# Performance work log

Measured on AMD Instinct MI355X. Metric: run time of the kernel, lower is better.

Reference implementation:

```python
import jax, jax.numpy as jnp
import numpy as np

B, P, C, SIZE, K = 2, 4096, 64, 128, 8
RADIUS_PX = 1.5
RAD_POW = 2
TAU = 1.0


def setup_inputs() -> dict:
    key = jax.random.key(0)
    k1, k2, k3 = jax.random.split(key, 3)
    xy = jax.random.uniform(k1, (B, P, 2), minval=-1.0, maxval=1.0)
    z = jax.random.uniform(k2, (B, P, 1), minval=0.1, maxval=2.0)
    pts3D = jnp.concatenate([xy, z], axis=-1)          # [B,P,3] NDC points, z>0
    src = jax.random.normal(k3, (B, C, P), dtype=jnp.float32)  # [B,C,P] features
    return {"pts3D": pts3D, "src": src}


def _rasterize_and_composite(pts3D, src):
    # flip x,y as in the original module (pytorch3d NDC: +x left, +y up)
    pts = pts3D * jnp.array([-1.0, -1.0, 1.0], dtype=pts3D.dtype)
    radius = RADIUS_PX / float(SIZE) * 2.0           # NDC radius
    # pixel-center NDC coordinates, [H,W]
    c = 1.0 - 2.0 * (jnp.arange(SIZE, dtype=pts.dtype) + 0.5) / SIZE
    grid_y, grid_x = jnp.meshgrid(c, c, indexing="ij")
    x, y, z = pts[..., 0], pts[..., 1], pts[..., 2]  # each [B,P]
    # squared NDC distance from every pixel to every point: [B,H,W,P]
    dx = grid_x[None, :, :, None] - x[:, None, None, :]
    dy = grid_y[None, :, :, None] - y[:, None, None, :]
    dist2 = dx * dx + dy * dy
    valid = (dist2 < radius * radius) & (z[:, None, None, :] > 0.0)
    zbuf = jnp.where(valid, z[:, None, None, :], jnp.inf)
    # k-buffer: K nearest-in-depth points per pixel
    neg_topz, idx = jax.lax.top_k(-zbuf, K)          # [B,H,W,K]
    points_idx = jnp.where(neg_topz > -jnp.inf, idx, -1)
    dists = jnp.take_along_axis(dist2, idx, axis=-1)  # [B,H,W,K]
    # blending weights
    dist_n = dists / (radius ** RAD_POW)
    alphas = (1.0 - jnp.clip(dist_n, 0.001, 1.0) ** 0.5) ** TAU
    alphas = jnp.where(points_idx >= 0, alphas, 0.0)
    # alpha compositing front-to-back: w_k = a_k * prod_{j<k} (1 - a_j)
    t = jnp.cumprod(1.0 - alphas, axis=-1)
    t_excl = jnp.concatenate([jnp.ones_like(t[..., :1]), t[..., :-1]], axis=-1)
    w = alphas * t_excl                               # [B,H,W,K]
    safe_idx = jnp.clip(points_idx, 0)
    feats = jax.vmap(lambda f, i: f[:, i])(src, safe_idx)  # [B,C,H,W,K]
    out = jnp.einsum("bchwk,bhwk->bchw", feats, w)
    return out, points_idx


def reference(pts3D, src):
    out, points_idx = _rasterize_and_composite(pts3D, src)
    # background mask: nearest slot empty, dilated by 3x3 max filter
    bg = (points_idx[..., 0] < 0).astype(jnp.float32)  # [B,H,W]
    bg = jax.lax.reduce_window(bg, -jnp.inf, jax.lax.max, (1, 3, 3), (1, 1, 1), "SAME") > 0
    return out, bg
```

## Files before the change

### kernel.cpp

```cpp
#include <hip/hip_runtime.h>
#include <math.h>

#define BB 2
#define PP 4096
#define CC 64
#define SZ 128
#define KK 8

#define R2f 0.00054931640625f
#define SLOTS 16
#define CG 16

typedef unsigned long long u64;
#define EMPTYK (~0ull)

__global__ __launch_bounds__(256) void prep_kernel(const float* __restrict__ pts,
                                                   const float* __restrict__ src,
                                                   float* __restrict__ srcT,
                                                   int* __restrict__ cnt,
                                                   u64* __restrict__ keys) {
    const int tidb = threadIdx.x;
    const int blk  = blockIdx.x;

    {
        const int t  = blk * 256 + tidb;
        const int r  = t & 3;
        const int gp = t >> 2;
        const int b  = gp >> 12;
        const int p  = gp & (PP - 1);
        const float px = pts[(size_t)gp * 3 + 0];
        const float py = pts[(size_t)gp * 3 + 1];
        const float pz = pts[(size_t)gp * 3 + 2];
        if (pz > 0.0f) {
            const float u = (1.0f + px) * 64.0f - 0.5f;
            const float v = (1.0f + py) * 64.0f - 0.5f;
            const int wlo = max(0,   (int)ceilf (u - 1.53f));
            const int whi = min(127, (int)floorf(u + 1.53f));
            const int hlo = max(0,   (int)ceilf (v - 1.53f));
            const int hhi = min(127, (int)floorf(v + 1.53f));
            const int h = hlo + r;
            if (h <= hhi && wlo <= whi) {
                const float gy  = 1.0f - (2 * h + 1) * (1.0f / 128.0f);
                const float dy  = __fadd_rn(gy, py);
                const float dy2 = __fmul_rn(dy, dy);
                const u64 zkey = ((u64)__float_as_uint(pz) << 32) | (unsigned)p;
                for (int w = wlo; w <= whi; ++w) {
                    const float gx = 1.0f - (2 * w + 1) * (1.0f / 128.0f);
                    const float dx = __fadd_rn(gx, px);
                    const float d2 = __fadd_rn(__fmul_rn(dx, dx), dy2);
                    if (d2 < R2f) {
                        const int pix = (b << 14) | (h << 7) | w;
                        const int pos = atomicAdd(cnt + pix, 1);
                        if (pos < SLOTS) keys[pix * SLOTS + pos] = zkey;
                    }
                }
            }
        }
    }

    __shared__ float lt[64][65];
    const int b2 = blk >> 6;
    const int p0 = (blk & 63) << 6;
    const int rr = tidb >> 6;
    const int cc = tidb & 63;
#pragma unroll
    for (int k = 0; k < 16; ++k) {
        const int c = k * 4 + rr;
        lt[c][cc] = src[(size_t)((b2 * CC + c) << 12 | (p0 + cc))];
    }
    __syncthreads();
#pragma unroll
    for (int k = 0; k < 16; ++k) {
        const int pl = k * 4 + rr;
        srcT[(size_t)(((b2 << 12) | (p0 + pl)) << 6 | cc)] = lt[cc][pl];
    }
}

__global__ __launch_bounds__(256) void selcomp_kernel(const float* __restrict__ pts,
                                                      const float* __restrict__ srcT,
                                                      const int* __restrict__ cnt,
                                                      const u64* __restrict__ keys,
                                                      float* __restrict__ out,
                                                      float* __restrict__ bgout) {
    const int t    = blockIdx.x * 256 + threadIdx.x;
    const int pix  = t & 16383;
    const int cg   = (t >> 14) & 3;
    const int b    = t >> 16;
    const int gpix = (b << 14) | pix;

    int n = cnt[gpix];
    n = (n > SLOTS) ? SLOTS : n;

    u64 kk[KK];
#pragma unroll
    for (int s = 0; s < KK; ++s) kk[s] = EMPTYK;
    for (int j = 0; j < n; ++j) {
        u64 kn = keys[gpix * SLOTS + j];
#pragma unroll
        for (int s = 0; s < KK; ++s) {
            if (kn < kk[s]) { u64 tk = kk[s]; kk[s] = kn; kn = tk; }
        }
    }

    const int w = pix & 127;
    const int h = pix >> 7;
    const float gx = 1.0f - (2 * w + 1) * (1.0f / 128.0f);
    const float gy = 1.0f - (2 * h + 1) * (1.0f / 128.0f);

    float acc[CG];
#pragma unroll
    for (int c = 0; c < CG; ++c) acc[c] = 0.0f;

    float T = 1.0f;
#pragma unroll
    for (int s = 0; s < KK; ++s) {
        if (kk[s] == EMPTYK) break;
        const int id = (int)(kk[s] & 0xffffffffu);
        const float* q = pts + (size_t)((b << 12) + id) * 3;
        const float dx = __fadd_rn(gx, q[0]);
        const float dy = __fadd_rn(gy, q[1]);
        const float d2 = __fadd_rn(__fmul_rn(dx, dx), __fmul_rn(dy, dy));
        float dn = d2 / R2f;
        dn = fminf(fmaxf(dn, 0.001f), 1.0f);
        const float a  = 1.0f - sqrtf(dn);
        const float wt = a * T;
        T = T * (1.0f - a);
        const float* fp = srcT + ((size_t)((b << 12) + id) << 6) + cg * CG;
#pragma unroll
        for (int v4 = 0; v4 < CG / 4; ++v4) {
            const float4 f = *(const float4*)(fp + v4 * 4);
            acc[v4 * 4 + 0] = fmaf(wt, f.x, acc[v4 * 4 + 0]);
            acc[v4 * 4 + 1] = fmaf(wt, f.y, acc[v4 * 4 + 1]);
            acc[v4 * 4 + 2] = fmaf(wt, f.z, acc[v4 * 4 + 2]);
            acc[v4 * 4 + 3] = fmaf(wt, f.w, acc[v4 * 4 + 3]);
        }
    }
#pragma unroll
    for (int c = 0; c < CG; ++c)
        out[((size_t)(b * CC + cg * CG + c) << 14) | pix] = acc[c];

    if (cg == 0) {
        int bgv = 0;
#pragma unroll
        for (int dh = -1; dh <= 1; ++dh)
#pragma unroll
            for (int dw = -1; dw <= 1; ++dw) {
                const int hh = h + dh, ww = w + dw;
                if (hh >= 0 && hh < 128 && ww >= 0 && ww < 128)
                    if (cnt[(b << 14) | (hh << 7) | ww] == 0) bgv = 1;
            }
        bgout[gpix] = bgv ? 1.0f : 0.0f;
    }
}

extern "C" void kernel_launch(void* const* d_in, const int* in_sizes, int n_in,
                              void* d_out, int out_size, void* d_ws, size_t ws_size,
                              hipStream_t stream) {
    const float* pts = (const float*)d_in[0];
    const float* src = (const float*)d_in[1];
    float* out = (float*)d_out;

    const int npix = BB * SZ * SZ;
    char* ws = (char*)d_ws;
    float* srcT = (float*)ws;
    int*   cnt  = (int*)(ws + (size_t)BB * PP * CC * 4);
    u64*   keys = (u64*)(ws + (size_t)BB * PP * CC * 4 + (size_t)npix * 4);

    hipMemsetAsync(cnt, 0, (size_t)npix * 4, stream);
    prep_kernel<<<128, 256, 0, stream>>>(pts, src, srcT, cnt, keys);
    selcomp_kernel<<<(BB * 4 * SZ * SZ) / 256, 256, 0, stream>>>(
        pts, srcT, cnt, keys, out, out + BB * CC * SZ * SZ);
}
```

Before: 27.08 us.

## Replace per-pixel append buffer with atomicMin sorted k-buffer insertion

```diff
diff --git a/kernel.cpp b/kernel.cpp
--- a/kernel.cpp
+++ b/kernel.cpp
@@ -8,98 +8,105 @@
 #define KK 8
 
 #define R2f 0.00054931640625f
-#define SLOTS 16
-#define CG 16
 
 typedef unsigned long long u64;
 #define EMPTYK (~0ull)
 
-__global__ __launch_bounds__(256) void prep_kernel(const float* __restrict__ pts,
-                                                   const float* __restrict__ src,
+__global__ __launch_bounds__(256) void prep_kernel(const float* __restrict__ src,
                                                    float* __restrict__ srcT,
-                                                   int* __restrict__ cnt,
                                                    u64* __restrict__ keys) {
     const int tidb = threadIdx.x;
     const int blk  = blockIdx.x;
+    if (blk < 128) {
+        __shared__ float lt[64][65];
+        const int b2  = blk >> 6;
+        const int p0  = (blk & 63) << 6;
+        const int rr  = tidb >> 6;
+        const int ccl = tidb & 63;
+#pragma unroll
+        for (int k = 0; k < 16; ++k) {
+            const int c = k * 4 + rr;
+            lt[c][ccl] = src[(size_t)((b2 * CC + c) << 12 | (p0 + ccl))];
+        }
+        __syncthreads();
+#pragma unroll
+        for (int k = 0; k < 16; ++k) {
+            const int pl = k * 4 + rr;
+            srcT[(size_t)(((b2 << 12) | (p0 + pl)) << 6 | ccl)] = lt[ccl][pl];
+        }
+    } else {
+        const int base = (blk - 128) * 256 + tidb;
+        for (int i = base; i < BB * SZ * SZ * KK; i += 384 * 256)
+            keys[i] = EMPTYK;
+    }
+}
 
-    {
-        const int t  = blk * 256 + tidb;
-        const int r  = t & 3;
-        const int gp = t >> 2;
-        const int b  = gp >> 12;
-        const int p  = gp & (PP - 1);
-        const float px = pts[(size_t)gp * 3 + 0];
-        const float py = pts[(size_t)gp * 3 + 1];
-        const float pz = pts[(size_t)gp * 3 + 2];
-        if (pz > 0.0f) {
-            const float u = (1.0f + px) * 64.0f - 0.5f;
-            const float v = (1.0f + py) * 64.0f - 0.5f;
-            const int wlo = max(0,   (int)ceilf (u - 1.53f));
-            const int whi = min(127, (int)floorf(u + 1.53f));
-            const int hlo = max(0,   (int)ceilf (v - 1.53f));
-            const int hhi = min(127, (int)floorf(v + 1.53f));
-            const int h = hlo + r;
-            if (h <= hhi && wlo <= whi) {
-                const float gy  = 1.0f - (2 * h + 1) * (1.0f / 128.0f);
-                const float dy  = __fadd_rn(gy, py);
-                const float dy2 = __fmul_rn(dy, dy);
-                const u64 zkey = ((u64)__float_as_uint(pz) << 32) | (unsigned)p;
-                for (int w = wlo; w <= whi; ++w) {
-                    const float gx = 1.0f - (2 * w + 1) * (1.0f / 128.0f);
-                    const float dx = __fadd_rn(gx, px);
-                    const float d2 = __fadd_rn(__fmul_rn(dx, dx), dy2);
-                    if (d2 < R2f) {
-                        const int pix = (b << 14) | (h << 7) | w;
-                        const int pos = atomicAdd(cnt + pix, 1);
-                        if (pos < SLOTS) keys[pix * SLOTS + pos] = zkey;
-                    }
-                }
+__global__ __launch_bounds__(256) void bin_kernel(const float* __restrict__ pts,
+                                                  u64* __restrict__ keys) {
+    const int t  = blockIdx.x * 256 + threadIdx.x;
+    const int r  = t & 3;
+    const int gp = t >> 2;
+    const int b  = gp >> 12;
+    const int p  = gp & (PP - 1);
+    const float px = pts[(size_t)gp * 3 + 0];
+    const float py = pts[(size_t)gp * 3 + 1];
+    const float pz = pts[(size_t)gp * 3 + 2];
+    if (!(pz > 0.0f)) return;
+    const float u = (1.0f + px) * 64.0f - 0.5f;
+    const float v = (1.0f + py) * 64.0f - 0.5f;
+    const int wlo = max(0,   (int)ceilf (u - 1.53f));
+    const int whi = min(127, (int)floorf(u + 1.53f));
+    const int hlo = max(0,   (int)ceilf (v - 1.53f));
+    const int hhi = min(127, (int)floorf(v + 1.53f));
+    const int h = hlo + r;
+    if (h > hhi || wlo > whi) return;
+
+    const float gy  = 1.0f - (2 * h + 1) * (1.0f / 128.0f);
+    const float dy  = __fadd_rn(gy, py);
+    const float dy2 = __fmul_rn(dy, dy);
+    const u64 zkey = ((u64)__float_as_uint(pz) << 32) | (unsigned)p;
+
+    for (int w = wlo; w <= whi; ++w) {
+        const float gx = 1.0f - (2 * w + 1) * (1.0f / 128.0f);
+        const float dx = __fadd_rn(gx, px);
+        const float d2 = __fadd_rn(__fmul_rn(dx, dx), dy2);
+        if (d2 < R2f) {
+            const int pix = (b << 14) | (h << 7) | w;
+            u64 kn = zkey;
+#pragma unroll
+            for (int s = 0; s < KK; ++s) {
+                const u64 old = atomicMin(&keys[(size_t)pix * KK + s], kn);
+                kn = (old > kn) ? old : kn;
+                if (kn == EMPTYK) break;
             }
         }
-    }
-
-    __shared__ float lt[64][65];
-    const int b2 = blk >> 6;
-    const int p0 = (blk & 63) << 6;
-    const int rr = tidb >> 6;
-    const int cc = tidb & 63;
-#pragma unroll
-    for (int k = 0; k < 16; ++k) {
-        const int c = k * 4 + rr;
-        lt[c][cc] = src[(size_t)((b2 * CC + c) << 12 | (p0 + cc))];
-    }
-    __syncthreads();
-#pragma unroll
-    for (int k = 0; k < 16; ++k) {
-        const int pl = k * 4 + rr;
-        srcT[(size_t)(((b2 << 12) | (p0 + pl)) << 6 | cc)] = lt[cc][pl];
     }
 }
 
 __global__ __launch_bounds__(256) void selcomp_kernel(const float* __restrict__ pts,
                                                       const float* __restrict__ srcT,
-                                                      const int* __restrict__ cnt,
                                                       const u64* __restrict__ keys,
                                                       float* __restrict__ out,
                                                       float* __restrict__ bgout) {
-    const int t    = blockIdx.x * 256 + threadIdx.x;
-    const int pix  = t & 16383;
-    const int cg   = (t >> 14) & 3;
-    const int b    = t >> 16;
+    const int blk = blockIdx.x;
+    const int ll  = threadIdx.x & 63;
+    const int cqi = threadIdx.x >> 6;
+    const int cqg = blk & 3;
+    const int pg  = (blk >> 2) & 255;
+    const int b   = blk >> 10;
+    const int cq  = cqg * 4 + cqi;
+    const int pix = pg * 64 + ll;
     const int gpix = (b << 14) | pix;
 
-    int n = cnt[gpix];
-    n = (n > SLOTS) ? SLOTS : n;
-
+    const u64* kp = keys + (size_t)gpix * KK;
     u64 kk[KK];
-#pragma unroll
-    for (int s = 0; s < KK; ++s) kk[s] = EMPTYK;
-    for (int j = 0; j < n; ++j) {
-        u64 kn = keys[gpix * SLOTS + j];
-#pragma unroll
-        for (int s = 0; s < KK; ++s) {
-            if (kn < kk[s]) { u64 tk = kk[s]; kk[s] = kn; kn = tk; }
-        }
+    {
+        const ulonglong2 k0 = *(const ulonglong2*)(kp + 0);
+        const ulonglong2 k1 = *(const ulonglong2*)(kp + 2);
+        const ulonglong2 k2 = *(const ulonglong2*)(kp + 4);
+        const ulonglong2 k3 = *(const ulonglong2*)(kp + 6);
+        kk[0] = k0.x; kk[1] = k0.y; kk[2] = k1.x; kk[3] = k1.y;
+        kk[4] = k2.x; kk[5] = k2.y; kk[6] = k3.x; kk[7] = k3.y;
     }
 
     const int w = pix & 127;
@@ -107,10 +114,7 @@
     const float gx = 1.0f - (2 * w + 1) * (1.0f / 128.0f);
     const float gy = 1.0f - (2 * h + 1) * (1.0f / 128.0f);
 
-    float acc[CG];
-#pragma unroll
-    for (int c = 0; c < CG; ++c) acc[c] = 0.0f;
-
+    float acc0 = 0.0f, acc1 = 0.0f, acc2 = 0.0f, acc3 = 0.0f;
     float T = 1.0f;
 #pragma unroll
     for (int s = 0; s < KK; ++s) {
@@ -125,21 +129,19 @@
         const float a  = 1.0f - sqrtf(dn);
         const float wt = a * T;
         T = T * (1.0f - a);
-        const float* fp = srcT + ((size_t)((b << 12) + id) << 6) + cg * CG;
-#pragma unroll
-        for (int v4 = 0; v4 < CG / 4; ++v4) {
-            const float4 f = *(const float4*)(fp + v4 * 4);
-            acc[v4 * 4 + 0] = fmaf(wt, f.x, acc[v4 * 4 + 0]);
-            acc[v4 * 4 + 1] = fmaf(wt, f.y, acc[v4 * 4 + 1]);
-            acc[v4 * 4 + 2] = fmaf(wt, f.z, acc[v4 * 4 + 2]);
-            acc[v4 * 4 + 3] = fmaf(wt, f.w, acc[v4 * 4 + 3]);
-        }
+        const float4 f = *(const float4*)(srcT + ((size_t)((b << 12) + id) << 6) + cq * 4);
+        acc0 = fmaf(wt, f.x, acc0);
+        acc1 = fmaf(wt, f.y, acc1);
+        acc2 = fmaf(wt, f.z, acc2);
+        acc3 = fmaf(wt, f.w, acc3);
     }
-#pragma unroll
-    for (int c = 0; c < CG; ++c)
-        out[((size_t)(b * CC + cg * CG + c) << 14) | pix] = acc[c];
+    const int c0 = cq * 4;
+    out[((size_t)(b * CC + c0 + 0) << 14) | pix] = acc0;
+    out[((size_t)(b * CC + c0 + 1) << 14) | pix] = acc1;
+    out[((size_t)(b * CC + c0 + 2) << 14) | pix] = acc2;
+    out[((size_t)(b * CC + c0 + 3) << 14) | pix] = acc3;
 
-    if (cg == 0) {
+    if (cqg == 0 && cqi == 0) {
         int bgv = 0;
 #pragma unroll
         for (int dh = -1; dh <= 1; ++dh)
@@ -147,7 +149,8 @@
             for (int dw = -1; dw <= 1; ++dw) {
                 const int hh = h + dh, ww = w + dw;
                 if (hh >= 0 && hh < 128 && ww >= 0 && ww < 128)
-                    if (cnt[(b << 14) | (hh << 7) | ww] == 0) bgv = 1;
+                    if (keys[(size_t)((b << 14) | (hh << 7) | ww) * KK] == EMPTYK)
+                        bgv = 1;
             }
         bgout[gpix] = bgv ? 1.0f : 0.0f;
     }
@@ -159,15 +162,13 @@
     const float* pts = (const float*)d_in[0];
     const float* src = (const float*)d_in[1];
     float* out = (float*)d_out;
+    float* bgout = out + BB * CC * SZ * SZ;
 
-    const int npix = BB * SZ * SZ;
     char* ws = (char*)d_ws;
     float* srcT = (float*)ws;
-    int*   cnt  = (int*)(ws + (size_t)BB * PP * CC * 4);
-    u64*   keys = (u64*)(ws + (size_t)BB * PP * CC * 4 + (size_t)npix * 4);
+    u64*   keys = (u64*)(ws + (size_t)BB * PP * CC * 4);
 
-    hipMemsetAsync(cnt, 0, (size_t)npix * 4, stream);
-    prep_kernel<<<128, 256, 0, stream>>>(pts, src, srcT, cnt, keys);
-    selcomp_kernel<<<(BB * 4 * SZ * SZ) / 256, 256, 0, stream>>>(
-        pts, srcT, cnt, keys, out, out + BB * CC * SZ * SZ);
+    prep_kernel<<<512, 256, 0, stream>>>(src, srcT, keys);
+    bin_kernel<<<(BB * PP * 4) / 256, 256, 0, stream>>>(pts, keys);
+    selcomp_kernel<<<2048, 256, 0, stream>>>(pts, srcT, keys, out, bgout);
 }
```

New measurement: 30.60 us. +13.0%, slower.

## Split prep into separate scatter and transpose blocks, widen composite parallelism

Applied to the files above, without the earlier changes.

```diff
diff --git a/kernel.cpp b/kernel.cpp
--- a/kernel.cpp
+++ b/kernel.cpp
@@ -9,7 +9,6 @@
 
 #define R2f 0.00054931640625f
 #define SLOTS 16
-#define CG 16
 
 typedef unsigned long long u64;
 #define EMPTYK (~0ull)
@@ -22,7 +21,7 @@
     const int tidb = threadIdx.x;
     const int blk  = blockIdx.x;
 
-    {
+    if (blk < 128) {
         const int t  = blk * 256 + tidb;
         const int r  = t & 3;
         const int gp = t >> 2;
@@ -31,48 +30,51 @@
         const float px = pts[(size_t)gp * 3 + 0];
         const float py = pts[(size_t)gp * 3 + 1];
         const float pz = pts[(size_t)gp * 3 + 2];
-        if (pz > 0.0f) {
-            const float u = (1.0f + px) * 64.0f - 0.5f;
-            const float v = (1.0f + py) * 64.0f - 0.5f;
-            const int wlo = max(0,   (int)ceilf (u - 1.53f));
-            const int whi = min(127, (int)floorf(u + 1.53f));
-            const int hlo = max(0,   (int)ceilf (v - 1.53f));
-            const int hhi = min(127, (int)floorf(v + 1.53f));
-            const int h = hlo + r;
-            if (h <= hhi && wlo <= whi) {
-                const float gy  = 1.0f - (2 * h + 1) * (1.0f / 128.0f);
-                const float dy  = __fadd_rn(gy, py);
-                const float dy2 = __fmul_rn(dy, dy);
-                const u64 zkey = ((u64)__float_as_uint(pz) << 32) | (unsigned)p;
-                for (int w = wlo; w <= whi; ++w) {
-                    const float gx = 1.0f - (2 * w + 1) * (1.0f / 128.0f);
-                    const float dx = __fadd_rn(gx, px);
-                    const float d2 = __fadd_rn(__fmul_rn(dx, dx), dy2);
-                    if (d2 < R2f) {
-                        const int pix = (b << 14) | (h << 7) | w;
-                        const int pos = atomicAdd(cnt + pix, 1);
-                        if (pos < SLOTS) keys[pix * SLOTS + pos] = zkey;
-                    }
-                }
+        if (!(pz > 0.0f)) return;
+        const float u = (1.0f + px) * 64.0f - 0.5f;
+        const float v = (1.0f + py) * 64.0f - 0.5f;
+        const int wlo = max(0,   (int)ceilf (u - 1.53f));
+        const int whi = min(127, (int)floorf(u + 1.53f));
+        const int hlo = max(0,   (int)ceilf (v - 1.53f));
+        const int hhi = min(127, (int)floorf(v + 1.53f));
+        const int h = hlo + r;
+        if (h > hhi || wlo > whi) return;
+        const float gy  = 1.0f - (2 * h + 1) * (1.0f / 128.0f);
+        const float dy  = __fadd_rn(gy, py);
+        const float dy2 = __fmul_rn(dy, dy);
+        const u64 zkey = ((u64)__float_as_uint(pz) << 32) | (unsigned)p;
+        for (int w = wlo; w <= whi; ++w) {
+            const float gx = 1.0f - (2 * w + 1) * (1.0f / 128.0f);
+            const float dx = __fadd_rn(gx, px);
+            const float d2 = __fadd_rn(__fmul_rn(dx, dx), dy2);
+            if (d2 < R2f) {
+                const int pix = (b << 14) | (h << 7) | w;
+                const int pos = atomicAdd(cnt + pix, 1);
+                if (pos < SLOTS) keys[(size_t)pix * SLOTS + pos] = zkey;
             }
         }
-    }
-
-    __shared__ float lt[64][65];
-    const int b2 = blk >> 6;
-    const int p0 = (blk & 63) << 6;
-    const int rr = tidb >> 6;
-    const int cc = tidb & 63;
+    } else {
+        __shared__ float lt[32][65];
+        const int tb  = blk - 128;
+        const int b2  = tb >> 7;
+        const int rem = tb & 127;
+        const int p0  = (rem >> 1) << 6;
+        const int c0  = (rem & 1) << 5;
+        const int rr  = tidb >> 6;
+        const int ccl = tidb & 63;
 #pragma unroll
-    for (int k = 0; k < 16; ++k) {
-        const int c = k * 4 + rr;
-        lt[c][cc] = src[(size_t)((b2 * CC + c) << 12 | (p0 + cc))];
-    }
-    __syncthreads();
+        for (int k = 0; k < 8; ++k) {
+            const int c = k * 4 + rr;
+            lt[c][ccl] = src[(size_t)((b2 * CC + c0 + c) << 12 | (p0 + ccl))];
+        }
+        __syncthreads();
+        const int cch = tidb & 31;
+        const int pl0 = tidb >> 5;
 #pragma unroll
-    for (int k = 0; k < 16; ++k) {
-        const int pl = k * 4 + rr;
-        srcT[(size_t)(((b2 << 12) | (p0 + pl)) << 6 | cc)] = lt[cc][pl];
+        for (int k = 0; k < 8; ++k) {
+            const int pl = pl0 + k * 8;
+            srcT[(size_t)(((b2 << 12) | (p0 + pl)) << 6) + c0 + cch] = lt[cch][pl];
+        }
     }
 }
 
@@ -84,21 +86,44 @@
                                                       float* __restrict__ bgout) {
     const int t    = blockIdx.x * 256 + threadIdx.x;
     const int pix  = t & 16383;
-    const int cg   = (t >> 14) & 3;
-    const int b    = t >> 16;
+    const int cg   = (t >> 14) & 7;
+    const int b    = t >> 17;
     const int gpix = (b << 14) | pix;
 
     int n = cnt[gpix];
     n = (n > SLOTS) ? SLOTS : n;
 
+    const u64* kp = keys + (size_t)gpix * SLOTS;
+    const ulonglong2 k01 = *(const ulonglong2*)(kp + 0);
+    const ulonglong2 k23 = *(const ulonglong2*)(kp + 2);
+
     u64 kk[KK];
 #pragma unroll
     for (int s = 0; s < KK; ++s) kk[s] = EMPTYK;
-    for (int j = 0; j < n; ++j) {
-        u64 kn = keys[gpix * SLOTS + j];
+#define INSK(KN) { u64 kn = (KN); \
+    _Pragma("unroll") for (int s = 0; s < KK; ++s) \
+        if (kn < kk[s]) { u64 tk = kk[s]; kk[s] = kn; kn = tk; } }
+    if (0 < n) INSK(k01.x);
+    if (1 < n) INSK(k01.y);
+    if (2 < n) INSK(k23.x);
+    if (3 < n) INSK(k23.y);
+    for (int j = 4; j < n; ++j) INSK(kp[j]);
+#undef INSK
+
+    const int nv = (n < KK) ? n : KK;
+
+    float qx[KK], qy[KK];
+    float4 f0[KK], f1[KK];
 #pragma unroll
-        for (int s = 0; s < KK; ++s) {
-            if (kn < kk[s]) { u64 tk = kk[s]; kk[s] = kn; kn = tk; }
+    for (int s = 0; s < KK; ++s) {
+        if (s < nv) {
+            const int id = (int)(kk[s] & 0xffffffffu);
+            const float* q = pts + (size_t)((b << 12) + id) * 3;
+            qx[s] = q[0];
+            qy[s] = q[1];
+            const float* fp = srcT + ((size_t)((b << 12) + id) << 6) + cg * 8;
+            f0[s] = *(const float4*)fp;
+            f1[s] = *(const float4*)(fp + 4);
         }
     }
 
@@ -107,37 +132,34 @@
     const float gx = 1.0f - (2 * w + 1) * (1.0f / 128.0f);
     const float gy = 1.0f - (2 * h + 1) * (1.0f / 128.0f);
 
-    float acc[CG];
+    float acc[8];
 #pragma unroll
-    for (int c = 0; c < CG; ++c) acc[c] = 0.0f;
-
+    for (int c = 0; c < 8; ++c) acc[c] = 0.0f;
     float T = 1.0f;
 #pragma unroll
     for (int s = 0; s < KK; ++s) {
-        if (kk[s] == EMPTYK) break;
-        const int id = (int)(kk[s] & 0xffffffffu);
-        const float* q = pts + (size_t)((b << 12) + id) * 3;
-        const float dx = __fadd_rn(gx, q[0]);
-        const float dy = __fadd_rn(gy, q[1]);
-        const float d2 = __fadd_rn(__fmul_rn(dx, dx), __fmul_rn(dy, dy));
-        float dn = d2 / R2f;
-        dn = fminf(fmaxf(dn, 0.001f), 1.0f);
-        const float a  = 1.0f - sqrtf(dn);
-        const float wt = a * T;
-        T = T * (1.0f - a);
-        const float* fp = srcT + ((size_t)((b << 12) + id) << 6) + cg * CG;
-#pragma unroll
-        for (int v4 = 0; v4 < CG / 4; ++v4) {
-            const float4 f = *(const float4*)(fp + v4 * 4);
-            acc[v4 * 4 + 0] = fmaf(wt, f.x, acc[v4 * 4 + 0]);
-            acc[v4 * 4 + 1] = fmaf(wt, f.y, acc[v4 * 4 + 1]);
-            acc[v4 * 4 + 2] = fmaf(wt, f.z, acc[v4 * 4 + 2]);
-            acc[v4 * 4 + 3] = fmaf(wt, f.w, acc[v4 * 4 + 3]);
+        if (s < nv) {
+            const float dx = __fadd_rn(gx, qx[s]);
+            const float dy = __fadd_rn(gy, qy[s]);
+            const float d2 = __fadd_rn(__fmul_rn(dx, dx), __fmul_rn(dy, dy));
+            float dn = d2 / R2f;
+            dn = fminf(fmaxf(dn, 0.001f), 1.0f);
+            const float a  = 1.0f - sqrtf(dn);
+            const float wt = a * T;
+            T = T * (1.0f - a);
+            acc[0] = fmaf(wt, f0[s].x, acc[0]);
+            acc[1] = fmaf(wt, f0[s].y, acc[1]);
+            acc[2] = fmaf(wt, f0[s].z, acc[2]);
+            acc[3] = fmaf(wt, f0[s].w, acc[3]);
+            acc[4] = fmaf(wt, f1[s].x, acc[4]);
+            acc[5] = fmaf(wt, f1[s].y, acc[5]);
+            acc[6] = fmaf(wt, f1[s].z, acc[6]);
+            acc[7] = fmaf(wt, f1[s].w, acc[7]);
         }
     }
 #pragma unroll
-    for (int c = 0; c < CG; ++c)
-        out[((size_t)(b * CC + cg * CG + c) << 14) | pix] = acc[c];
+    for (int c = 0; c < 8; ++c)
+        out[((size_t)(b * CC + cg * 8 + c) << 14) | pix] = acc[c];
 
     if (cg == 0) {
         int bgv = 0;
@@ -159,6 +181,7 @@
     const float* pts = (const float*)d_in[0];
     const float* src = (const float*)d_in[1];
     float* out = (float*)d_out;
+    float* bgout = out + BB * CC * SZ * SZ;
 
     const int npix = BB * SZ * SZ;
     char* ws = (char*)d_ws;
@@ -167,7 +190,7 @@
     u64*   keys = (u64*)(ws + (size_t)BB * PP * CC * 4 + (size_t)npix * 4);
 
     hipMemsetAsync(cnt, 0, (size_t)npix * 4, stream);
-    prep_kernel<<<128, 256, 0, stream>>>(pts, src, srcT, cnt, keys);
-    selcomp_kernel<<<(BB * 4 * SZ * SZ) / 256, 256, 0, stream>>>(
-        pts, srcT, cnt, keys, out, out + BB * CC * SZ * SZ);
+    prep_kernel<<<384, 256, 0, stream>>>(pts, src, srcT, cnt, keys);
+    selcomp_kernel<<<(BB * 8 * SZ * SZ) / 256, 256, 0, stream>>>(
+        pts, srcT, cnt, keys, out, bgout);
 }
```

Result: faster. 26.32 us (-2.8%).
